# Performance work log

Hardware: AMD Instinct MI355X
Metric: run time of the kernel (lower is better)

## Reference

```python
import jax, jax.numpy as jnp
import numpy as np

B, C, H, W = 8, 16, 512, 512


def setup_inputs() -> dict:
    key = jax.random.key(0)
    kx, kr, ki = jax.random.split(key, 3)
    x = jax.random.normal(kx, (B, C, H, W), dtype=jnp.float32)
    H_real = jax.random.normal(kr, (H, W), dtype=jnp.float32)
    H_imag = jax.random.normal(ki, (H, W), dtype=jnp.float32)
    return {"x": x, "H_real": H_real, "H_imag": H_imag}


def reference(x, H_real, H_imag):
    # FFT over the last two (spatial) dims, pointwise complex filter, inverse FFT.
    x_fft = jnp.fft.fft2(x)                       # [B,C,H,W] complex64
    H_complex = jax.lax.complex(H_real, H_imag)   # [H,W] complex64, broadcasts
    y = jnp.fft.ifft2(x_fft * H_complex)
    return jnp.real(y)
```

## Files before the change

### kernel.cpp

```cpp
#include <hip/hip_runtime.h>
#include <hip/hip_fp16.h>

__device__ __forceinline__ float2 cmul(float2 a, float2 b) {
    return make_float2(a.x*b.x - a.y*b.y, a.x*b.y + a.y*b.x);
}
__device__ __forceinline__ float2 cadd(float2 a, float2 b){ return make_float2(a.x+b.x, a.y+b.y); }
__device__ __forceinline__ float2 csub(float2 a, float2 b){ return make_float2(a.x-b.x, a.y-b.y); }

__device__ __forceinline__ void wsync() {
    asm volatile("s_waitcnt lgkmcnt(0)" ::: "memory");
}

template<int SGN> __device__ __forceinline__ float2 mul_i(float2 a) {
    return (SGN > 0) ? make_float2(-a.y, a.x) : make_float2(a.y, -a.x);
}
template<int SGN> __device__ __forceinline__ float2 mul_w81(float2 a) {
    const float r = 0.70710678118654752440f;
    return (SGN > 0) ? make_float2(r*(a.x - a.y), r*(a.x + a.y))
                     : make_float2(r*(a.x + a.y), r*(a.y - a.x));
}
template<int SGN> __device__ __forceinline__ float2 mul_w83(float2 a) {
    const float r = 0.70710678118654752440f;
    return (SGN > 0) ? make_float2(-r*(a.x + a.y), r*(a.x - a.y))
                     : make_float2(r*(a.y - a.x), -r*(a.x + a.y));
}

template<int SGN>
__device__ __forceinline__ void bfly8(float2 v[8]) {
    float2 s0 = cadd(v[0], v[4]), d0 = csub(v[0], v[4]);
    float2 s1 = cadd(v[1], v[5]), d1 = csub(v[1], v[5]);
    float2 s2 = cadd(v[2], v[6]), d2 = csub(v[2], v[6]);
    float2 s3 = cadd(v[3], v[7]), d3 = csub(v[3], v[7]);
    d1 = mul_w81<SGN>(d1);
    d2 = mul_i<SGN>(d2);
    d3 = mul_w83<SGN>(d3);
    float2 p0 = cadd(s0, s2), q0 = csub(s0, s2);
    float2 p1 = cadd(s1, s3), q1 = mul_i<SGN>(csub(s1, s3));
    float2 P0 = cadd(d0, d2), Q0 = csub(d0, d2);
    float2 P1 = cadd(d1, d3), Q1 = mul_i<SGN>(csub(d1, d3));
    v[0] = cadd(p0, p1);
    v[4] = csub(p0, p1);
    v[2] = cadd(q0, q1);
    v[6] = csub(q0, q1);
    v[1] = cadd(P0, P1);
    v[5] = csub(P0, P1);
    v[3] = cadd(Q0, Q1);
    v[7] = csub(Q0, Q1);
}

template<int SGN>
__device__ __forceinline__ void twiddle7(float2 v[8], float frac) {
    const float ang = (SGN > 0 ? 6.2831853071795864769f : -6.2831853071795864769f) * frac;
    float sn, cs; __sincosf(ang, &sn, &cs);
    const float2 w1 = make_float2(cs, sn);
    float2 w = w1;
    v[1] = cmul(v[1], w);
#pragma unroll
    for (int q = 2; q < 8; ++q) { w = cmul(w, w1); v[q] = cmul(v[q], w); }
}

__device__ __forceinline__ void fft512_fwd(float2 v[8], float2* S, int l) {
    const int g = l >> 3, j = l & 7;
    bfly8<-1>(v);
    twiddle7<-1>(v, (float)l * (1.0f/512.0f));
#pragma unroll
    for (int q = 0; q < 8; ++q) S[66*q + l] = v[q];
    wsync();
#pragma unroll
    for (int k = 0; k < 8; ++k) v[k] = S[66*g + j + 8*k];
    bfly8<-1>(v);
    twiddle7<-1>(v, (float)j * (1.0f/64.0f));
#pragma unroll
    for (int q = 0; q < 8; ++q) S[72*g + 9*q + j] = v[q];
    wsync();
#pragma unroll
    for (int k = 0; k < 8; ++k) v[k] = S[9*l + k];
    bfly8<-1>(v);
}

__device__ __forceinline__ void fft512_inv(float2 v[8], float2* S, int l) {
    const int g = l >> 3, j = l & 7;
    bfly8<1>(v);
#pragma unroll
    for (int k = 0; k < 8; ++k) S[9*l + k] = v[k];
    wsync();
#pragma unroll
    for (int q = 0; q < 8; ++q) v[q] = S[72*g + 9*q + j];
    twiddle7<1>(v, (float)j * (1.0f/64.0f));
    bfly8<1>(v);
#pragma unroll
    for (int k = 0; k < 8; ++k) S[66*g + j + 8*k] = v[k];
    wsync();
#pragma unroll
    for (int q = 0; q < 8; ++q) v[q] = S[66*q + l];
    twiddle7<1>(v, (float)l * (1.0f/512.0f));
    bfly8<1>(v);
}

__device__ __forceinline__ int drev(int x) {
    return ((x & 7) << 6) | (x & 56) | (x >> 6);
}


__global__ __launch_bounds__(256) void pass1_rows(const float* __restrict__ x,
                                                  __half2* __restrict__ ws,
                                                  const float* __restrict__ Hr,
                                                  const float* __restrict__ Hi,
                                                  float2* __restrict__ Hp) {
    if (blockIdx.x < 512) {
        const int pw = blockIdx.x;
        const int kw = drev(pw);
        const int nw = (512 - kw) & 511;
        const float s = 0.5f / (512.0f * 512.0f);
        for (int ph = threadIdx.x; ph < 512; ph += 256) {
            const int kh = drev(ph);
            const int nh = (512 - kh) & 511;
            const float hr = s * (Hr[(kh << 9) + kw] + Hr[(nh << 9) + nw]);
            const float hi = s * (Hi[(kh << 9) + kw] - Hi[(nh << 9) + nw]);
            Hp[(pw << 9) + ph] = make_float2(hr, hi);
        }
        return;
    }
    __shared__ float2 smem[4 * 577];
    const int t = threadIdx.x;
    const int l = t & 63, w = t >> 6;
    float2* S = smem + w * 577;
    const size_t row = (size_t)(blockIdx.x - 512) * 4 + w;
    const size_t img = row >> 9;
    const size_t h   = row & 511;
    const float* src1 = x + ((img * 2) << 18) + (h << 9);
    const float* src2 = src1 + (1 << 18);
    float2 v[8];
#pragma unroll
    for (int k = 0; k < 8; ++k) v[k] = make_float2(src1[l + 64*k], src2[l + 64*k]);
    fft512_fwd(v, S, l);
    __half2 ob[8];
#pragma unroll
    for (int q = 0; q < 8; ++q) ob[q] = __float22half2_rn(v[q]);
    float4* dst = (float4*)(ws + row * 512 + 8*l);
    dst[0] = *(float4*)&ob[0];
    dst[1] = *(float4*)&ob[4];
}

__global__ __launch_bounds__(512) void pass2_cols(__half2* __restrict__ ws,
                                                  const float2* __restrict__ Hp) {
    __shared__ float2 smem[4616];
    const int t = threadIdx.x;
    const int l = t & 63, w = t >> 6;
    const int img = blockIdx.x >> 6;
    const int w0 = (blockIdx.x & 63) * 8;
    __half2* base = ws + ((size_t)img << 18) + w0;

    {
        const int c = t & 1, u = t >> 1;
#pragma unroll
        for (int k = 0; k < 2; ++k) {
            int h = u + 256*k;
            float4 p = *(const float4*)(base + (size_t)h * 512 + 4*c);
            const __half2* pp = (const __half2*)&p;
#pragma unroll
            for (int i = 0; i < 4; ++i)
                smem[9*h + 4*c + i] = __half22float2(pp[i]);
        }
    }
    __syncthreads();
    float2 v[8];
#pragma unroll
    for (int k = 0; k < 8; ++k) v[k] = smem[9*(l + 64*k) + w];
    __syncthreads();
    float2* S = smem + w * 577;
    fft512_fwd(v, S, l);
    {
        const float4* hp = (const float4*)(Hp + (((size_t)(w0 + w)) << 9) + 8*l);
#pragma unroll
        for (int q = 0; q < 4; ++q) {
            float4 h2 = hp[q];
            v[2*q]   = cmul(v[2*q],   make_float2(h2.x, h2.y));
            v[2*q+1] = cmul(v[2*q+1], make_float2(h2.z, h2.w));
        }
    }
    fft512_inv(v, S, l);
    __syncthreads();
#pragma unroll
    for (int k = 0; k < 8; ++k) smem[9*(l + 64*k) + w] = v[k];
    __syncthreads();
    {
        const int c = t & 1, u = t >> 1;
#pragma unroll
        for (int k = 0; k < 2; ++k) {
            int h = u + 256*k;
            __half2 ob[4];
#pragma unroll
            for (int i = 0; i < 4; ++i)
                ob[i] = __float22half2_rn(smem[9*h + 4*c + i]);
            *(float4*)(base + (size_t)h * 512 + 4*c) = *(float4*)&ob[0];
        }
    }
}

__global__ __launch_bounds__(256) void pass3_rows(const __half2* __restrict__ ws,
                                                  float* __restrict__ out) {
    __shared__ float2 smem[4 * 577];
    const int t = threadIdx.x;
    const int l = t & 63, w = t >> 6;
    float2* S = smem + w * 577;
    const size_t row = (size_t)blockIdx.x * 4 + w;
    const size_t img = row >> 9;
    const size_t h   = row & 511;
    const float4* src = (const float4*)(ws + row * 512 + 8*l);
    float4 a = src[0], b = src[1];
    float2 v[8];
    {
        const __half2* pa = (const __half2*)&a;
        const __half2* pb = (const __half2*)&b;
#pragma unroll
        for (int k = 0; k < 4; ++k) v[k]     = __half22float2(pa[k]);
#pragma unroll
        for (int k = 0; k < 4; ++k) v[4 + k] = __half22float2(pb[k]);
    }
    fft512_inv(v, S, l);
    float* dst1 = out + ((img * 2) << 18) + (h << 9);
    float* dst2 = dst1 + (1 << 18);
#pragma unroll
    for (int k = 0; k < 8; ++k) {
        dst1[l + 64*k] = v[k].x;
        dst2[l + 64*k] = v[k].y;
    }
}

extern "C" void kernel_launch(void* const* d_in, const int* in_sizes, int n_in,
                              void* d_out, int out_size, void* d_ws, size_t ws_size,
                              hipStream_t stream) {
    const float* x  = (const float*)d_in[0];
    const float* Hr = (const float*)d_in[1];
    const float* Hi = (const float*)d_in[2];
    float* out = (float*)d_out;
    __half2* ws = (__half2*)d_ws;
    float2* Hp = (float2*)((char*)d_ws + ((size_t)64 << 20));

    pass1_rows<<<8704, 256, 0, stream>>>(x, ws, Hr, Hi, Hp);
    pass2_cols<<<4096, 512, 0, stream>>>(ws, Hp);
    pass3_rows<<<8192, 256, 0, stream>>>(ws, out);
}
```

Baseline: 331.1 us.

## Process sixteen columns per block in column pass, staging fp16 in LDS

New measurement: 307.4 us. 7.2% less time.

```diff
diff --git a/kernel.cpp b/kernel.cpp
--- a/kernel.cpp
+++ b/kernel.cpp
@@ -145,54 +145,71 @@
 __global__ __launch_bounds__(512) void pass2_cols(__half2* __restrict__ ws,
                                                   const float2* __restrict__ Hp) {
     __shared__ float2 smem[4616];
+    __half2* sh = (__half2*)smem;
     const int t = threadIdx.x;
     const int l = t & 63, w = t >> 6;
-    const int img = blockIdx.x >> 6;
-    const int w0 = (blockIdx.x & 63) * 8;
+    const int img = blockIdx.x >> 5;
+    const int w0 = (blockIdx.x & 31) * 16;
     __half2* base = ws + ((size_t)img << 18) + w0;
 
     {
-        const int c = t & 1, u = t >> 1;
-#pragma unroll
-        for (int k = 0; k < 2; ++k) {
-            int h = u + 256*k;
+        const int c = t & 3, u = t >> 2;
+#pragma unroll
+        for (int k = 0; k < 4; ++k) {
+            int h = u + 128*k;
             float4 p = *(const float4*)(base + (size_t)h * 512 + 4*c);
             const __half2* pp = (const __half2*)&p;
 #pragma unroll
-            for (int i = 0; i < 4; ++i)
-                smem[9*h + 4*c + i] = __half22float2(pp[i]);
-        }
-    }
-    __syncthreads();
-    float2 v[8];
-#pragma unroll
-    for (int k = 0; k < 8; ++k) v[k] = smem[9*(l + 64*k) + w];
+            for (int i = 0; i < 4; ++i) sh[17*h + 4*c + i] = pp[i];
+        }
+    }
+    __syncthreads();
+    float2 va[8], vb[8];
+    const int c0 = 2*w, c1 = 2*w + 1;
+#pragma unroll
+    for (int k = 0; k < 8; ++k) {
+        va[k] = __half22float2(sh[17*(l + 64*k) + c0]);
+        vb[k] = __half22float2(sh[17*(l + 64*k) + c1]);
+    }
     __syncthreads();
     float2* S = smem + w * 577;
-    fft512_fwd(v, S, l);
-    {
-        const float4* hp = (const float4*)(Hp + (((size_t)(w0 + w)) << 9) + 8*l);
+    fft512_fwd(va, S, l);
+    {
+        const float4* hp = (const float4*)(Hp + (((size_t)(w0 + c0)) << 9) + 8*l);
 #pragma unroll
         for (int q = 0; q < 4; ++q) {
             float4 h2 = hp[q];
-            v[2*q]   = cmul(v[2*q],   make_float2(h2.x, h2.y));
-            v[2*q+1] = cmul(v[2*q+1], make_float2(h2.z, h2.w));
-        }
-    }
-    fft512_inv(v, S, l);
-    __syncthreads();
-#pragma unroll
-    for (int k = 0; k < 8; ++k) smem[9*(l + 64*k) + w] = v[k];
-    __syncthreads();
-    {
-        const int c = t & 1, u = t >> 1;
-#pragma unroll
-        for (int k = 0; k < 2; ++k) {
-            int h = u + 256*k;
+            va[2*q]   = cmul(va[2*q],   make_float2(h2.x, h2.y));
+            va[2*q+1] = cmul(va[2*q+1], make_float2(h2.z, h2.w));
+        }
+    }
+    fft512_inv(va, S, l);
+    fft512_fwd(vb, S, l);
+    {
+        const float4* hp = (const float4*)(Hp + (((size_t)(w0 + c1)) << 9) + 8*l);
+#pragma unroll
+        for (int q = 0; q < 4; ++q) {
+            float4 h2 = hp[q];
+            vb[2*q]   = cmul(vb[2*q],   make_float2(h2.x, h2.y));
+            vb[2*q+1] = cmul(vb[2*q+1], make_float2(h2.z, h2.w));
+        }
+    }
+    fft512_inv(vb, S, l);
+    __syncthreads();
+#pragma unroll
+    for (int k = 0; k < 8; ++k) {
+        sh[17*(l + 64*k) + c0] = __float22half2_rn(va[k]);
+        sh[17*(l + 64*k) + c1] = __float22half2_rn(vb[k]);
+    }
+    __syncthreads();
+    {
+        const int c = t & 3, u = t >> 2;
+#pragma unroll
+        for (int k = 0; k < 4; ++k) {
+            int h = u + 128*k;
             __half2 ob[4];
 #pragma unroll
-            for (int i = 0; i < 4; ++i)
-                ob[i] = __float22half2_rn(smem[9*h + 4*c + i]);
+            for (int i = 0; i < 4; ++i) ob[i] = sh[17*h + 4*c + i];
             *(float4*)(base + (size_t)h * 512 + 4*c) = *(float4*)&ob[0];
         }
     }
@@ -239,6 +256,6 @@
     float2* Hp = (float2*)((char*)d_ws + ((size_t)64 << 20));
 
     pass1_rows<<<8704, 256, 0, stream>>>(x, ws, Hr, Hi, Hp);
-    pass2_cols<<<4096, 512, 0, stream>>>(ws, Hp);
+    pass2_cols<<<2048, 512, 0, stream>>>(ws, Hp);
     pass3_rows<<<8192, 256, 0, stream>>>(ws, out);
 }
```
